# Kernel tuning notes

Hardware: AMD Instinct MI355X
Metric: run time of the kernel (lower is better)

The kernel has to match this reference:

```python
import jax, jax.numpy as jnp
import numpy as np

KH = KW = 3
PAD = 1
SPE = 16  # msfa 4x4

def _unfold(x):
    # torch F.unfold order: feature index = c*(kh*kw) + di*kw + dj
    N, C, H, W = x.shape
    xp = jnp.pad(x, ((0, 0), (0, 0), (PAD, PAD), (PAD, PAD)))
    patches = jnp.stack(
        [xp[:, :, di:di + H, dj:dj + W] for di in range(KH) for dj in range(KW)],
        axis=2,
    )  # [N, C, KH*KW, H, W]
    return patches.reshape(N, C * KH * KW, H * W)

def setup_inputs() -> dict:
    key = jax.random.key(0)
    k1, k2 = jax.random.split(key)
    x = jax.random.normal(k1, (4, 32, 256, 256), dtype=jnp.float32)
    # kaiming_uniform(a=sqrt(5)) on fan_in = in_channels*kh*kw of the (spe,K,outC) tensor;
    # exact init distribution is irrelevant for correctness baseline, use scaled uniform.
    fan_in = 288
    bound = np.sqrt(6.0 / ((1 + 5) * fan_in))
    weight = jax.random.uniform(k2, (SPE, 288, 64), dtype=jnp.float32, minval=-bound, maxval=bound)
    return {"x": x, "weight": weight}

def reference(x, weight):
    N, C, H, W = x.shape
    spe, K, outC = weight.shape  # (16, 288, 64)
    cols = _unfold(x)                      # [N, K, HW]
    cols = jnp.transpose(cols, (0, 2, 1))  # [N, HW, K]
    G = (H * W) // spe
    colsg = cols.reshape(N, G, spe, K)     # position p uses weight[p % spe]
    out = jnp.einsum('ngsk,skc->ngsc', colsg, weight)  # [N, G, spe, outC]
    out = out.reshape(N, H, W, outC).transpose(0, 3, 1, 2)  # [N, outC, H, W]
    return out
```

## Files before the change

kernel.cpp:

```cpp
#include <hip/hip_runtime.h>
#include <hip/hip_bf16.h>


using bf16 = __hip_bfloat16;
typedef __attribute__((ext_vector_type(8))) short bf16x8_t;
typedef __attribute__((ext_vector_type(4))) float f32x4_t;

constexpr int NB    = 4;
constexpr int C_IN  = 32;
constexpr int HH    = 256;
constexpr int WW    = 256;
constexpr int C_OUT = 64;
constexpr int SPE   = 16;

constexpr int TH = 16;
constexpr int TW = 32;
constexpr int XR = TH + 2;
constexpr int XC = TW + 2;
constexpr int CPAD = 40;

__global__ __launch_bounds__(256)
void prep_weights(const float* __restrict__ w, bf16* __restrict__ wt) {
    int idx = blockIdx.x * 256 + threadIdx.x;
    if (idx >= SPE * C_OUT * 288) return;
    int s  = idx / (C_OUT * 288);
    int r  = idx % (C_OUT * 288);
    int co = r / 288;
    int kk = r % 288;
    int tap = kk >> 5;
    int c   = kk & 31;
    float v = w[((size_t)s * 288 + c * 9 + tap) * C_OUT + co];
    wt[idx] = __float2bfloat16(v);
}

__global__ __launch_bounds__(1024, 4)
void conv_mosaic_mfma(const float* __restrict__ x,
                      const bf16* __restrict__ wt,
                      float* __restrict__ out) {
    __shared__ __align__(16) bf16 xs[XR * XC * CPAD];

    const int n  = blockIdx.y;
    const int tw = blockIdx.x & 7;
    const int th = blockIdx.x >> 3;
    const int h0 = th * TH;
    const int w0 = tw * TW;
    const int t  = threadIdx.x;

    const float* xn = x + (size_t)n * C_IN * HH * WW;
    constexpr int VJOBS = C_IN * XR * 8;
#pragma unroll
    for (int it = 0; it < 5; ++it) {
        const int idx = t + it * 1024;
        if (idx < VJOBS) {
            const int c  = idx / (XR * 8);
            const int rr = idx % (XR * 8);
            const int r  = rr >> 3;
            const int q  = rr & 7;
            const int gh = h0 + r - 1;
            float4 v = make_float4(0.f, 0.f, 0.f, 0.f);
            if (gh >= 0 && gh < HH)
                v = *reinterpret_cast<const float4*>(
                    &xn[((size_t)c * HH + gh) * WW + w0 + q * 4]);
            bf16* d = &xs[(r * XC + q * 4 + 1) * CPAD + c];
            d[0]        = __float2bfloat16(v.x);
            d[CPAD]     = __float2bfloat16(v.y);
            d[2 * CPAD] = __float2bfloat16(v.z);
            d[3 * CPAD] = __float2bfloat16(v.w);
        }
    }
    constexpr int EJOBS = C_IN * XR * 2;
#pragma unroll
    for (int it = 0; it < 2; ++it) {
        const int idx = t + it * 1024;
        if (idx < EJOBS) {
            const int c   = idx / (XR * 2);
            const int rr  = idx % (XR * 2);
            const int r   = rr >> 1;
            const int e   = rr & 1;
            const int col = e ? 33 : 0;
            const int gh  = h0 + r - 1;
            const int gw  = w0 + (e ? 32 : -1);
            float vv = 0.f;
            if (gh >= 0 && gh < HH && gw >= 0 && gw < WW)
                vv = xn[((size_t)c * HH + gh) * WW + gw];
            xs[(r * XC + col) * CPAD + c] = __float2bfloat16(vv);
        }
    }
    __syncthreads();

    const int wave = t >> 6;
    const int lane = t & 63;
    const int g    = wave & 3;
    const int ct   = wave >> 2;
    const int lm   = lane & 15;
    const int lg   = lane >> 4;

    f32x4_t dacc[2][4];
#pragma unroll
    for (int b = 0; b < 2; ++b)
#pragma unroll
        for (int c = 0; c < 4; ++c) dacc[b][c] = (f32x4_t){0.f, 0.f, 0.f, 0.f};

#pragma unroll
    for (int si = 0; si < 4; ++si) {
        const int s = g * 4 + si;
        const bf16* bp = wt + ((size_t)(s * C_OUT + ct * 16 + lm) * 288 + lg * 8);
        bf16x8_t bfr[9];
#pragma unroll
        for (int tap = 0; tap < 9; ++tap)
            bfr[tap] = *reinterpret_cast<const bf16x8_t*>(bp + tap * 32);

        const bf16* ap = &xs[(lm * XC + s) * CPAD + lg * 8];
#pragma unroll
        for (int tap = 0; tap < 9; ++tap) {
            const int di = tap / 3, dj = tap % 3;
            bf16x8_t a0 = *reinterpret_cast<const bf16x8_t*>(ap + (di * XC + dj) * CPAD);
            bf16x8_t a1 = *reinterpret_cast<const bf16x8_t*>(ap + (di * XC + dj + 16) * CPAD);
            dacc[0][si] = __builtin_amdgcn_mfma_f32_16x16x32_bf16(a0, bfr[tap], dacc[0][si], 0, 0, 0);
            dacc[1][si] = __builtin_amdgcn_mfma_f32_16x16x32_bf16(a1, bfr[tap], dacc[1][si], 0, 0, 0);
        }
    }

    const int co = ct * 16 + lm;
#pragma unroll
    for (int wm = 0; wm < 2; ++wm) {
#pragma unroll
        for (int j = 0; j < 4; ++j) {
            const int h = h0 + lg * 4 + j;
            float4 v = make_float4(dacc[wm][0][j], dacc[wm][1][j],
                                   dacc[wm][2][j], dacc[wm][3][j]);
            *reinterpret_cast<float4*>(
                &out[(((size_t)n * C_OUT + co) * HH + h) * WW + w0 + g * 4 + wm * 16]) = v;
        }
    }
}

extern "C" void kernel_launch(void* const* d_in, const int* in_sizes, int n_in,
                              void* d_out, int out_size, void* d_ws, size_t ws_size,
                              hipStream_t stream) {
    const float* x = (const float*)d_in[0];
    const float* w = (const float*)d_in[1];
    float* out     = (float*)d_out;
    bf16* wt       = (bf16*)d_ws;

    prep_weights<<<(SPE * C_OUT * 288 + 255) / 256, 256, 0, stream>>>(w, wt);

    dim3 grid((WW / TW) * (HH / TH), NB);
    conv_mosaic_mfma<<<grid, 1024, 0, stream>>>(x, wt, out);
}
```

Baseline: 62.53 us.

## Switch to 32x32x16 MFMA with taller tiles and lane-packed weight layout

Replaces the 16x16x32 bf16 MFMA path with 32x32x16 MFMA, so each wave computes 32 rows by 32 output channels per spectral slot. The tile becomes 32x16 with 512-thread blocks, and the shared row stride is padded to 19 columns to spread LDS bank accesses. Weights are pre-permuted into a per-lane fragment layout so B loads are contiguous 16-byte reads. The aim is fewer MFMA issues and loads per FLOP; the cost is a larger halo fraction per tile and more accumulator registers.

```diff
diff --git a/kernel.cpp b/kernel.cpp
--- a/kernel.cpp
+++ b/kernel.cpp
@@ -4,7 +4,7 @@
 
 using bf16 = __hip_bfloat16;
 typedef __attribute__((ext_vector_type(8))) short bf16x8_t;
-typedef __attribute__((ext_vector_type(4))) float f32x4_t;
+typedef __attribute__((ext_vector_type(16))) float f32x16_t;
 
 constexpr int NB    = 4;
 constexpr int C_IN  = 32;
@@ -13,55 +13,66 @@
 constexpr int C_OUT = 64;
 constexpr int SPE   = 16;
 
-constexpr int TH = 16;
-constexpr int TW = 32;
-constexpr int XR = TH + 2;
-constexpr int XC = TW + 2;
+constexpr int TH  = 32;
+constexpr int TW  = 16;
+constexpr int XR  = TH + 2;
+constexpr int XC  = TW + 2;
+constexpr int XCL = 19;
 constexpr int CPAD = 40;
 
 __global__ __launch_bounds__(256)
-void prep_weights(const float* __restrict__ w, bf16* __restrict__ wt) {
-    int idx = blockIdx.x * 256 + threadIdx.x;
-    if (idx >= SPE * C_OUT * 288) return;
-    int s  = idx / (C_OUT * 288);
-    int r  = idx % (C_OUT * 288);
-    int co = r / 288;
-    int kk = r % 288;
-    int tap = kk >> 5;
-    int c   = kk & 31;
-    float v = w[((size_t)s * 288 + c * 9 + tap) * C_OUT + co];
-    wt[idx] = __float2bfloat16(v);
+void prep_weights(const float* __restrict__ w, bf16* __restrict__ wt3) {
+    int o = blockIdx.x * 256 + threadIdx.x;
+    if (o >= SPE * 2 * 9 * 2 * 64 * 8) return;
+    int v   = o & 7;
+    int l   = (o >> 3) & 63;
+    int kh  = (o >> 9) & 1;
+    int r   = o >> 10;
+    int tap = r % 9;
+    int sc  = r / 9;
+    int ct2 = sc & 1;
+    int s   = sc >> 1;
+    int c   = kh * 16 + (l >> 5) * 8 + v;
+    int co  = ct2 * 32 + (l & 31);
+    wt3[o] = __float2bfloat16(w[((size_t)s * 288 + c * 9 + tap) * C_OUT + co]);
 }
 
-__global__ __launch_bounds__(1024, 4)
+__global__ __launch_bounds__(512, 4)
 void conv_mosaic_mfma(const float* __restrict__ x,
-                      const bf16* __restrict__ wt,
+                      const bf16* __restrict__ wt3,
                       float* __restrict__ out) {
-    __shared__ __align__(16) bf16 xs[XR * XC * CPAD];
+    __shared__ __align__(16) bf16 xs[XR * XCL * CPAD];
 
     const int n  = blockIdx.y;
-    const int tw = blockIdx.x & 7;
-    const int th = blockIdx.x >> 3;
+    const int tw = blockIdx.x & 15;
+    const int th = blockIdx.x >> 4;
     const int h0 = th * TH;
     const int w0 = tw * TW;
     const int t  = threadIdx.x;
 
+    const int wave = t >> 6;
+    const int lane = t & 63;
+    const int g    = wave & 3;
+    const int ct2  = wave >> 2;
+    const int lr   = lane & 31;
+    const int lk   = lane >> 5;
+
     const float* xn = x + (size_t)n * C_IN * HH * WW;
-    constexpr int VJOBS = C_IN * XR * 8;
+    constexpr int VJOBS = C_IN * XR * 4;
 #pragma unroll
-    for (int it = 0; it < 5; ++it) {
-        const int idx = t + it * 1024;
+    for (int it = 0; it < 9; ++it) {
+        const int idx = t + it * 512;
         if (idx < VJOBS) {
-            const int c  = idx / (XR * 8);
-            const int rr = idx % (XR * 8);
-            const int r  = rr >> 3;
-            const int q  = rr & 7;
+            const int c  = idx / (XR * 4);
+            const int rr = idx % (XR * 4);
+            const int r  = rr >> 2;
+            const int q  = rr & 3;
             const int gh = h0 + r - 1;
             float4 v = make_float4(0.f, 0.f, 0.f, 0.f);
             if (gh >= 0 && gh < HH)
                 v = *reinterpret_cast<const float4*>(
                     &xn[((size_t)c * HH + gh) * WW + w0 + q * 4]);
-            bf16* d = &xs[(r * XC + q * 4 + 1) * CPAD + c];
+            bf16* d = &xs[(r * XCL + q * 4 + 1) * CPAD + c];
             d[0]        = __float2bfloat16(v.x);
             d[CPAD]     = __float2bfloat16(v.y);
             d[2 * CPAD] = __float2bfloat16(v.z);
@@ -70,68 +81,60 @@
     }
     constexpr int EJOBS = C_IN * XR * 2;
 #pragma unroll
-    for (int it = 0; it < 2; ++it) {
-        const int idx = t + it * 1024;
+    for (int it = 0; it < 5; ++it) {
+        const int idx = t + it * 512;
         if (idx < EJOBS) {
             const int c   = idx / (XR * 2);
             const int rr  = idx % (XR * 2);
             const int r   = rr >> 1;
             const int e   = rr & 1;
-            const int col = e ? 33 : 0;
+            const int col = e ? (XC - 1) : 0;
             const int gh  = h0 + r - 1;
-            const int gw  = w0 + (e ? 32 : -1);
+            const int gw  = w0 + (e ? TW : -1);
             float vv = 0.f;
             if (gh >= 0 && gh < HH && gw >= 0 && gw < WW)
                 vv = xn[((size_t)c * HH + gh) * WW + gw];
-            xs[(r * XC + col) * CPAD + c] = __float2bfloat16(vv);
+            xs[(r * XCL + col) * CPAD + c] = __float2bfloat16(vv);
         }
     }
     __syncthreads();
 
-    const int wave = t >> 6;
-    const int lane = t & 63;
-    const int g    = wave & 3;
-    const int ct   = wave >> 2;
-    const int lm   = lane & 15;
-    const int lg   = lane >> 4;
-
-    f32x4_t dacc[2][4];
+    f32x16_t dacc[4];
 #pragma unroll
-    for (int b = 0; b < 2; ++b)
+    for (int si = 0; si < 4; ++si)
 #pragma unroll
-        for (int c = 0; c < 4; ++c) dacc[b][c] = (f32x4_t){0.f, 0.f, 0.f, 0.f};
+        for (int j = 0; j < 16; ++j) dacc[si][j] = 0.f;
 
 #pragma unroll
     for (int si = 0; si < 4; ++si) {
         const int s = g * 4 + si;
-        const bf16* bp = wt + ((size_t)(s * C_OUT + ct * 16 + lm) * 288 + lg * 8);
-        bf16x8_t bfr[9];
+        const bf16* bp = wt3 + (size_t)(s * 2 + ct2) * 9216 + lane * 8;
+        const bf16* ap = &xs[(lr * XCL + s) * CPAD + lk * 8];
 #pragma unroll
-        for (int tap = 0; tap < 9; ++tap)
-            bfr[tap] = *reinterpret_cast<const bf16x8_t*>(bp + tap * 32);
-
-        const bf16* ap = &xs[(lm * XC + s) * CPAD + lg * 8];
+        for (int kh = 0; kh < 2; ++kh) {
+            bf16x8_t bfr[9];
 #pragma unroll
-        for (int tap = 0; tap < 9; ++tap) {
-            const int di = tap / 3, dj = tap % 3;
-            bf16x8_t a0 = *reinterpret_cast<const bf16x8_t*>(ap + (di * XC + dj) * CPAD);
-            bf16x8_t a1 = *reinterpret_cast<const bf16x8_t*>(ap + (di * XC + dj + 16) * CPAD);
-            dacc[0][si] = __builtin_amdgcn_mfma_f32_16x16x32_bf16(a0, bfr[tap], dacc[0][si], 0, 0, 0);
-            dacc[1][si] = __builtin_amdgcn_mfma_f32_16x16x32_bf16(a1, bfr[tap], dacc[1][si], 0, 0, 0);
+            for (int tap = 0; tap < 9; ++tap)
+                bfr[tap] = *reinterpret_cast<const bf16x8_t*>(bp + (tap * 2 + kh) * 512);
+            __builtin_amdgcn_sched_barrier(0);
+#pragma unroll
+            for (int tap = 0; tap < 9; ++tap) {
+                const int di = tap / 3, dj = tap % 3;
+                bf16x8_t a = *reinterpret_cast<const bf16x8_t*>(
+                    ap + (di * XCL + dj) * CPAD + kh * 16);
+                dacc[si] = __builtin_amdgcn_mfma_f32_32x32x16_bf16(
+                    a, bfr[tap], dacc[si], 0, 0, 0);
+            }
         }
     }
 
-    const int co = ct * 16 + lm;
+    const int co = ct2 * 32 + lr;
 #pragma unroll
-    for (int wm = 0; wm < 2; ++wm) {
-#pragma unroll
-        for (int j = 0; j < 4; ++j) {
-            const int h = h0 + lg * 4 + j;
-            float4 v = make_float4(dacc[wm][0][j], dacc[wm][1][j],
-                                   dacc[wm][2][j], dacc[wm][3][j]);
-            *reinterpret_cast<float4*>(
-                &out[(((size_t)n * C_OUT + co) * HH + h) * WW + w0 + g * 4 + wm * 16]) = v;
-        }
+    for (int j = 0; j < 16; ++j) {
+        const int h = h0 + (j & 3) + 8 * (j >> 2) + 4 * lk;
+        float4 v = make_float4(dacc[0][j], dacc[1][j], dacc[2][j], dacc[3][j]);
+        *reinterpret_cast<float4*>(
+            &out[(((size_t)n * C_OUT + co) * HH + h) * WW + w0 + g * 4]) = v;
     }
 }
 
@@ -141,10 +144,10 @@
     const float* x = (const float*)d_in[0];
     const float* w = (const float*)d_in[1];
     float* out     = (float*)d_out;
-    bf16* wt       = (bf16*)d_ws;
+    bf16* wt3      = (bf16*)d_ws;
 
-    prep_weights<<<(SPE * C_OUT * 288 + 255) / 256, 256, 0, stream>>>(w, wt);
+    prep_weights<<<(SPE * 2 * 9 * 2 * 64 * 8 + 255) / 256, 256, 0, stream>>>(w, wt3);
 
     dim3 grid((WW / TW) * (HH / TH), NB);
-    conv_mosaic_mfma<<<grid, 1024, 0, stream>>>(x, wt, out);
+    conv_mosaic_mfma<<<grid, 512, 0, stream>>>(x, wt3, out);
 }
```

After: 67.61 us. 1.08x slower.

## Halve tile height, use 512-thread blocks, reuse A fragments across two channel tiles

Applied to the files above, without the earlier changes.

Tile height drops from 16 to 8 rows and blocks shrink to 512 threads, which gives twice as many blocks and allows higher occupancy. Each wave now loads nine A fragments per spectral position once and reuses them across two output-channel tiles, streaming B weights per tap. The output store changes from float4 vectors to scalar stores per pixel, strided by 16 columns, so write coalescing gets worse. Halo overhead per output pixel also grows with the smaller tile.

```diff
diff --git a/kernel.cpp b/kernel.cpp
--- a/kernel.cpp
+++ b/kernel.cpp
@@ -13,7 +13,7 @@
 constexpr int C_OUT = 64;
 constexpr int SPE   = 16;
 
-constexpr int TH = 16;
+constexpr int TH = 8;
 constexpr int TW = 32;
 constexpr int XR = TH + 2;
 constexpr int XC = TW + 2;
@@ -33,7 +33,7 @@
     wt[idx] = __float2bfloat16(v);
 }
 
-__global__ __launch_bounds__(1024, 4)
+__global__ __launch_bounds__(512, 8)
 void conv_mosaic_mfma(const float* __restrict__ x,
                       const bf16* __restrict__ wt,
                       float* __restrict__ out) {
@@ -50,7 +50,7 @@
     constexpr int VJOBS = C_IN * XR * 8;
 #pragma unroll
     for (int it = 0; it < 5; ++it) {
-        const int idx = t + it * 1024;
+        const int idx = t + it * 512;
         if (idx < VJOBS) {
             const int c  = idx / (XR * 8);
             const int rr = idx % (XR * 8);
@@ -71,7 +71,7 @@
     constexpr int EJOBS = C_IN * XR * 2;
 #pragma unroll
     for (int it = 0; it < 2; ++it) {
-        const int idx = t + it * 1024;
+        const int idx = t + it * 512;
         if (idx < EJOBS) {
             const int c   = idx / (XR * 2);
             const int rr  = idx % (XR * 2);
@@ -91,46 +91,44 @@
     const int wave = t >> 6;
     const int lane = t & 63;
     const int g    = wave & 3;
-    const int ct   = wave >> 2;
+    const int cth  = wave >> 2;
     const int lm   = lane & 15;
     const int lg   = lane >> 4;
 
-    f32x4_t dacc[2][4];
-#pragma unroll
-    for (int b = 0; b < 2; ++b)
-#pragma unroll
-        for (int c = 0; c < 4; ++c) dacc[b][c] = (f32x4_t){0.f, 0.f, 0.f, 0.f};
+    const int arow = lm & 7;
+    const int awh  = lm >> 3;
+    const int dh   = (lg & 1) * 4;
+    const int dwh  = lg >> 1;
 
 #pragma unroll
     for (int si = 0; si < 4; ++si) {
         const int s = g * 4 + si;
-        const bf16* bp = wt + ((size_t)(s * C_OUT + ct * 16 + lm) * 288 + lg * 8);
-        bf16x8_t bfr[9];
-#pragma unroll
-        for (int tap = 0; tap < 9; ++tap)
-            bfr[tap] = *reinterpret_cast<const bf16x8_t*>(bp + tap * 32);
 
-        const bf16* ap = &xs[(lm * XC + s) * CPAD + lg * 8];
+        bf16x8_t afr[9];
+        const bf16* ap = &xs[((arow) * XC + s + 16 * awh) * CPAD + lg * 8];
 #pragma unroll
         for (int tap = 0; tap < 9; ++tap) {
             const int di = tap / 3, dj = tap % 3;
-            bf16x8_t a0 = *reinterpret_cast<const bf16x8_t*>(ap + (di * XC + dj) * CPAD);
-            bf16x8_t a1 = *reinterpret_cast<const bf16x8_t*>(ap + (di * XC + dj + 16) * CPAD);
-            dacc[0][si] = __builtin_amdgcn_mfma_f32_16x16x32_bf16(a0, bfr[tap], dacc[0][si], 0, 0, 0);
-            dacc[1][si] = __builtin_amdgcn_mfma_f32_16x16x32_bf16(a1, bfr[tap], dacc[1][si], 0, 0, 0);
+            afr[tap] = *reinterpret_cast<const bf16x8_t*>(ap + (di * XC + dj) * CPAD);
         }
-    }
 
-    const int co = ct * 16 + lm;
 #pragma unroll
-    for (int wm = 0; wm < 2; ++wm) {
+        for (int ctl = 0; ctl < 2; ++ctl) {
+            const int ct = cth * 2 + ctl;
+            const bf16* bp = wt + ((size_t)(s * C_OUT + ct * 16 + lm) * 288 + lg * 8);
+            f32x4_t dacc = {0.f, 0.f, 0.f, 0.f};
 #pragma unroll
-        for (int j = 0; j < 4; ++j) {
-            const int h = h0 + lg * 4 + j;
-            float4 v = make_float4(dacc[wm][0][j], dacc[wm][1][j],
-                                   dacc[wm][2][j], dacc[wm][3][j]);
-            *reinterpret_cast<float4*>(
-                &out[(((size_t)n * C_OUT + co) * HH + h) * WW + w0 + g * 4 + wm * 16]) = v;
+            for (int tap = 0; tap < 9; ++tap) {
+                bf16x8_t bfr = *reinterpret_cast<const bf16x8_t*>(bp + tap * 32);
+                dacc = __builtin_amdgcn_mfma_f32_16x16x32_bf16(afr[tap], bfr, dacc, 0, 0, 0);
+            }
+            const int co = ct * 16 + lm;
+            const int w  = w0 + s + 16 * dwh;
+#pragma unroll
+            for (int j = 0; j < 4; ++j) {
+                const int h = h0 + dh + j;
+                out[(((size_t)n * C_OUT + co) * HH + h) * WW + w] = dacc[j];
+            }
         }
     }
 }
@@ -146,5 +144,5 @@
     prep_weights<<<(SPE * C_OUT * 288 + 255) / 256, 256, 0, stream>>>(w, wt);
 
     dim3 grid((WW / TW) * (HH / TH), NB);
-    conv_mosaic_mfma<<<grid, 1024, 0, stream>>>(x, wt, out);
+    conv_mosaic_mfma<<<grid, 512, 0, stream>>>(x, wt, out);
 }
```

New measurement: 85.44 us. +36.6%, slower.
